# Performance work log

Hardware: AMD Instinct MI355X
Metric: run time of the kernel (lower is better)

The kernel has to match this reference:

```python
import jax, jax.numpy as jnp
from jax import lax
import numpy as np

NUM_INPUTS = 512
NUM_HIDDENS = 1024
BATCH = 64
SEQ_LEN = 512


def setup_inputs() -> dict:
    key = jax.random.key(0)
    ks = jax.random.split(key, 8)
    D, H = NUM_INPUTS, NUM_HIDDENS
    w = lambda k, shape: 0.01 * jax.random.normal(k, shape, dtype=jnp.float32)
    return {
        "inputs": jax.random.normal(ks[0], (BATCH, SEQ_LEN, D), dtype=jnp.float32),
        "state": jax.random.normal(ks[1], (BATCH, H), dtype=jnp.float32),
        "W_xz": w(ks[2], (D, H)), "W_hz": w(ks[3], (H, H)), "b_z": jnp.zeros((H,), jnp.float32),
        "W_xr": w(ks[4], (D, H)), "W_hr": w(ks[5], (H, H)), "b_r": jnp.zeros((H,), jnp.float32),
        "W_xh": w(ks[6], (D, H)), "W_hh": w(ks[7], (H, H)), "b_h": jnp.zeros((H,), jnp.float32),
    }


def reference(inputs, state, W_xz, W_hz, b_z, W_xr, W_hr, b_r, W_xh, W_hh, b_h):
    B, T, _ = inputs.shape
    Hd = state.shape[1]
    # Precompute all input-side gate projections in three big GEMMs: [T, B, H]
    xz = (jnp.einsum('btd,dh->bth', inputs, W_xz) + b_z).transpose(1, 0, 2)
    xr = (jnp.einsum('btd,dh->bth', inputs, W_xr) + b_r).transpose(1, 0, 2)
    xh = (jnp.einsum('btd,dh->bth', inputs, W_xh) + b_h).transpose(1, 0, 2)

    def step(Hc, xs):
        xz_t, xr_t, xh_t = xs
        Z = jax.nn.sigmoid(xz_t + Hc @ W_hz)
        R = jax.nn.sigmoid(xr_t + Hc @ W_hr)
        H_tilda = jnp.tanh(xh_t + (R * Hc) @ W_hh)
        Hn = Z * Hc + (1.0 - Z) * H_tilda
        return Hn, Hn

    H_final, outs = lax.scan(step, state, (xz, xr, xh))  # outs: [T, B, H]
    # torch.cat(outputs, 0) -> [T*B, H]; .transpose(1, 0) -> [H, T*B]
    outputs = outs.reshape(T * B, Hd).T
    return outputs, H_final
```

## Files before the change

kernel.cpp:

```cpp
#include <hip/hip_runtime.h>
#include <hip/hip_bf16.h>

typedef unsigned short ushort_t;
typedef unsigned int uint32;
typedef unsigned long long ull;
typedef short bf16x8 __attribute__((ext_vector_type(8)));
typedef float f32x4 __attribute__((ext_vector_type(4)));

#define Bb 64
#define Tt 512
#define Dd 512
#define Hh 1024
#define KK 1536
#define KP 1544
#define NBLK 64
#define OUT2_OFF 33554432ull
#define FLAGS_OFF 9699328ull
#define XB_OFF    9707776ull
#define XB_BYTES  33554432ull


__device__ inline ushort_t f2b(float f) {
    __hip_bfloat16 h = __float2bfloat16(f);
    return __builtin_bit_cast(ushort_t, h);
}
__device__ inline float b2f(ushort_t u) {
    uint32 x = ((uint32)u) << 16;
    return __builtin_bit_cast(float, x);
}
__device__ inline bf16x8 ld_bf8(const ushort_t* p) {
    uint4 v = *reinterpret_cast<const uint4*>(p);
    return __builtin_bit_cast(bf16x8, v);
}
__device__ inline bf16x8 ld_x8(const float* p) {
    float4 u = *reinterpret_cast<const float4*>(p);
    float4 v = *reinterpret_cast<const float4*>(p + 4);
    bf16x8 a;
    a[0] = (short)f2b(u.x); a[1] = (short)f2b(u.y); a[2] = (short)f2b(u.z); a[3] = (short)f2b(u.w);
    a[4] = (short)f2b(v.x); a[5] = (short)f2b(v.y); a[6] = (short)f2b(v.z); a[7] = (short)f2b(v.w);
    return a;
}
__device__ inline bf16x8 ld_a8(const ushort_t* p) {
    union { ull q[2]; bf16x8 v; } u;
    u.q[0] = __hip_atomic_load((const ull*)p,       __ATOMIC_RELAXED, __HIP_MEMORY_SCOPE_AGENT);
    u.q[1] = __hip_atomic_load((const ull*)(p + 4), __ATOMIC_RELAXED, __HIP_MEMORY_SCOPE_AGENT);
    return u.v;
}
__device__ inline void st_a8(ushort_t* p, ull v) {
    __hip_atomic_store((ull*)p, v, __ATOMIC_RELAXED, __HIP_MEMORY_SCOPE_AGENT);
}

#define MFMA(a, b, c) __builtin_amdgcn_mfma_f32_16x16x32_bf16((a), (b), (c), 0, 0, 0)

__device__ inline void b_arrive(uint32* flags, uint32 val) {
    asm volatile("s_waitcnt vmcnt(0)" ::: "memory");
    __syncthreads();
    if (threadIdx.x == 0)
        __hip_atomic_store(flags + (uint32)blockIdx.x * 32, val,
                           __ATOMIC_RELAXED, __HIP_MEMORY_SCOPE_AGENT);
}
__device__ inline void b_wait(uint32* flags, uint32 val) {
    if (threadIdx.x < 64) {
        uint32 v;
        do {
            v = __hip_atomic_load(flags + threadIdx.x * 32,
                                  __ATOMIC_RELAXED, __HIP_MEMORY_SCOPE_AGENT);
        } while (__any((int)(v < val)));
    }
    __syncthreads();
    asm volatile("" ::: "memory");
}

__global__ __launch_bounds__(256) void k_init(const float* __restrict__ state,
                                              ushort_t* __restrict__ HB, uint32* flags) {
    int i = blockIdx.x * 256 + threadIdx.x;
    if (i < Bb * Hh) HB[i] = f2b(state[i]);
    if (i < 2112) flags[i] = 0;
}

__global__ __launch_bounds__(256) void k_xb(const float* __restrict__ inp,
                                            ushort_t* __restrict__ XB) {
    size_t i = ((size_t)blockIdx.x * 256 + threadIdx.x) * 8;
    bf16x8 v = ld_x8(inp + i);
    *reinterpret_cast<uint4*>(XB + i) = __builtin_bit_cast(uint4, v);
}

__global__ __launch_bounds__(256) void k_wt(const float* __restrict__ Wxz, const float* __restrict__ Whz,
                                            const float* __restrict__ Wxr, const float* __restrict__ Whr,
                                            const float* __restrict__ Wxh, const float* __restrict__ Whh,
                                            ushort_t* __restrict__ WT) {
    __shared__ float lds[64][65];
    int id = blockIdx.x;
    int g = id / 384, rem = id % 384, nt = rem / 24, kt = rem % 24;
    const float* Wx = (g == 0) ? Wxz : (g == 1) ? Wxr : Wxh;
    const float* Wh = (g == 0) ? Whz : (g == 1) ? Whr : Whh;
    int n0 = nt * 64, k0 = kt * 64;
    int tr = threadIdx.x >> 6, tc = threadIdx.x & 63;
    #pragma unroll
    for (int i = 0; i < 16; i++) {
        int kl = i * 4 + tr, k = k0 + kl;
        lds[kl][tc] = (k < 512) ? Wx[(size_t)k * Hh + n0 + tc]
                                : Wh[(size_t)(k - 512) * Hh + n0 + tc];
    }
    __syncthreads();
    #pragma unroll
    for (int i = 0; i < 16; i++) {
        int nl = i * 4 + tr;
        WT[((size_t)g * Hh + n0 + nl) * KK + k0 + tc] = f2b(lds[tc][nl]);
    }
}

__global__ __launch_bounds__(256, 1) void gru_persist(
    const float* __restrict__ inp, const ushort_t* __restrict__ XB, int use_xb,
    const float* __restrict__ bz, const float* __restrict__ br, const float* __restrict__ bh,
    ushort_t* HB, ushort_t* RH, const ushort_t* __restrict__ WT,
    uint32* flags, float* __restrict__ out) {
    __shared__ ushort_t WL[3 * 16 * KP];
    __shared__ ushort_t stage[4][256];

    const int bi = blockIdx.x;
    const int tid = threadIdx.x;

    for (int r = tid >> 4; r < 48; r += 16) {
        const ushort_t* src = WT + ((size_t)(r >> 4) * Hh + bi * 16 + (r & 15)) * KK;
        ushort_t* dst = WL + (size_t)r * KP;
        for (int c = tid & 15; c < 192; c += 16)
            *reinterpret_cast<uint4*>(dst + c * 8) = *reinterpret_cast<const uint4*>(src + c * 8);
    }

    const int l = tid & 63, w = tid >> 6;
    const int lrow = l & 15, lq = l >> 4;
    const int lk8 = lq << 3;

    const int arow = w * 16 + lrow;
    const int brow0 = w * 16 + lq * 4;
    const float*    xbF = inp + (size_t)arow * (Tt * Dd) + lk8;
    const ushort_t* xbB = XB + (size_t)arow * (Tt * Dd) + lk8;
    const ushort_t* hbase = HB + arow * Hh + lk8;
    const ushort_t* rbase = RH + arow * Hh + lk8;
    const int ncol = bi * 16 + lrow;
    const ushort_t* wlz = WL + (0 * 16 + lrow) * KP + lk8;
    const ushort_t* wlr = WL + (1 * 16 + lrow) * KP + lk8;
    const ushort_t* wlh = WL + (2 * 16 + lrow) * KP + lk8;
    const float bzv = bz[ncol], brv = br[ncol], bhv = bh[ncol];

    const size_t strow = (size_t)(w * 16 + (l >> 2)) * Hh + bi * 16 + (l & 3) * 4;
    ushort_t* stW = &stage[w][0];
    const int stw_off = (l >> 2) * 16 + (l & 3) * 4;

    float hold[4];
    #pragma unroll
    for (int j = 0; j < 4; j++) hold[j] = b2f(HB[(size_t)(brow0 + j) * Hh + ncol]);

    __syncthreads();

    for (int t = 0; t < Tt; ++t) {
        bf16x8 xa[16];
        if (use_xb) {
            const ushort_t* xp = xbB + (size_t)t * Dd;
            #pragma unroll
            for (int i = 0; i < 16; i++) xa[i] = ld_bf8(xp + i * 32);
        } else {
            const float* xp = xbF + (size_t)t * Dd;
            #pragma unroll
            for (int i = 0; i < 16; i++) xa[i] = ld_x8(xp + i * 32);
        }

        f32x4 az0 = {0,0,0,0}, az1 = {0,0,0,0}, ar0 = {0,0,0,0}, ar1 = {0,0,0,0};
        f32x4 ah0 = {0,0,0,0}, ah1 = {0,0,0,0}, ah2 = {0,0,0,0}, ah3 = {0,0,0,0};
        #pragma unroll
        for (int kk = 0; kk < 16; kk += 2) {
            const int o = kk * 32;
            az0 = MFMA(xa[kk],     ld_bf8(wlz + o),      az0);
            az1 = MFMA(xa[kk + 1], ld_bf8(wlz + o + 32), az1);
            ar0 = MFMA(xa[kk],     ld_bf8(wlr + o),      ar0);
            ar1 = MFMA(xa[kk + 1], ld_bf8(wlr + o + 32), ar1);
            ah0 = MFMA(xa[kk],     ld_bf8(wlh + o),      ah0);
            ah1 = MFMA(xa[kk + 1], ld_bf8(wlh + o + 32), ah1);
        }

        b_wait(flags, 2u * (uint32)t);

        #pragma unroll
        for (int kk = 0; kk < 32; kk += 2) {
            const int o = kk * 32;
            bf16x8 a0 = ld_a8(hbase + o);
            bf16x8 a1 = ld_a8(hbase + o + 32);
            az0 = MFMA(a0, ld_bf8(wlz + 512 + o),      az0);
            az1 = MFMA(a1, ld_bf8(wlz + 512 + o + 32), az1);
            ar0 = MFMA(a0, ld_bf8(wlr + 512 + o),      ar0);
            ar1 = MFMA(a1, ld_bf8(wlr + 512 + o + 32), ar1);
        }
        f32x4 az = az0 + az1, ar = ar0 + ar1;
        float zreg[4];
        #pragma unroll
        for (int j = 0; j < 4; j++) {
            float zz = 1.f / (1.f + __expf(-(az[j] + bzv)));
            float rr = 1.f / (1.f + __expf(-(ar[j] + brv)));
            zreg[j] = zz;
            stW[(lq * 4 + j) * 16 + lrow] = f2b(rr * hold[j]);
        }
        asm volatile("s_waitcnt lgkmcnt(0)" ::: "memory");
        st_a8(RH + strow, *reinterpret_cast<const ull*>(stW + stw_off));
        b_arrive(flags, 2u * (uint32)t + 1u);
        b_wait(flags, 2u * (uint32)t + 1u);

        #pragma unroll
        for (int kk = 0; kk < 32; kk += 4) {
            const int o = kk * 32;
            bf16x8 a0 = ld_a8(rbase + o);
            bf16x8 a1 = ld_a8(rbase + o + 32);
            bf16x8 a2 = ld_a8(rbase + o + 64);
            bf16x8 a3 = ld_a8(rbase + o + 96);
            ah0 = MFMA(a0, ld_bf8(wlh + 512 + o),      ah0);
            ah1 = MFMA(a1, ld_bf8(wlh + 512 + o + 32), ah1);
            ah2 = MFMA(a2, ld_bf8(wlh + 512 + o + 64), ah2);
            ah3 = MFMA(a3, ld_bf8(wlh + 512 + o + 96), ah3);
        }
        f32x4 ah = (ah0 + ah1) + (ah2 + ah3);
        float hn[4];
        #pragma unroll
        for (int j = 0; j < 4; j++) {
            float pre = ah[j] + bhv;
            float e = __expf(-2.f * fabsf(pre));
            float th = (1.f - e) / (1.f + e);
            th = copysignf(th, pre);
            float v = zreg[j] * hold[j] + (1.f - zreg[j]) * th;
            hold[j] = v;
            hn[j] = v;
            stW[(lq * 4 + j) * 16 + lrow] = f2b(v);
        }
        asm volatile("s_waitcnt lgkmcnt(0)" ::: "memory");
        st_a8(HB + strow, *reinterpret_cast<const ull*>(stW + stw_off));
        *reinterpret_cast<float4*>(out + (size_t)ncol * (Tt * Bb) + (size_t)t * Bb + brow0) =
            make_float4(hn[0], hn[1], hn[2], hn[3]);
        if (t == Tt - 1) {
            #pragma unroll
            for (int j = 0; j < 4; j++)
                out[OUT2_OFF + (size_t)(brow0 + j) * Hh + ncol] = hn[j];
        }
        b_arrive(flags, 2u * (uint32)t + 2u);
    }
}

extern "C" void kernel_launch(void* const* d_in, const int* in_sizes, int n_in,
                              void* d_out, int out_size, void* d_ws, size_t ws_size,
                              hipStream_t stream) {
    const float* inp   = (const float*)d_in[0];
    const float* state = (const float*)d_in[1];
    const float* Wxz   = (const float*)d_in[2];
    const float* Whz   = (const float*)d_in[3];
    const float* bz    = (const float*)d_in[4];
    const float* Wxr   = (const float*)d_in[5];
    const float* Whr   = (const float*)d_in[6];
    const float* br    = (const float*)d_in[7];
    const float* Wxh   = (const float*)d_in[8];
    const float* Whh   = (const float*)d_in[9];
    const float* bh    = (const float*)d_in[10];
    float* out = (float*)d_out;

    char* ws = (char*)d_ws;
    ushort_t* HB    = (ushort_t*)(ws);
    ushort_t* RH    = (ushort_t*)(ws + 131072);
    ushort_t* WT    = (ushort_t*)(ws + 262144);
    uint32*   flags = (uint32*)(ws + FLAGS_OFF);
    ushort_t* XB    = (ushort_t*)(ws + XB_OFF);
    int use_xb = (ws_size >= XB_OFF + XB_BYTES) ? 1 : 0;

    k_init<<<dim3(256), dim3(256), 0, stream>>>(state, HB, flags);
    k_wt<<<dim3(1152), dim3(256), 0, stream>>>(Wxz, Whz, Wxr, Whr, Wxh, Whh, WT);
    if (use_xb)
        k_xb<<<dim3(8192), dim3(256), 0, stream>>>(inp, XB);

    void* args[] = {(void*)&inp, (void*)&XB, (void*)&use_xb,
                    (void*)&bz, (void*)&br, (void*)&bh,
                    (void*)&HB, (void*)&RH, (void*)&WT, (void*)&flags, (void*)&out};
    hipError_t e = hipLaunchCooperativeKernel((const void*)gru_persist, dim3(NBLK), dim3(256),
                                              args, 0, stream);
    if (e != hipSuccess) {
        gru_persist<<<dim3(NBLK), dim3(256), 0, stream>>>(inp, XB, use_xb, bz, br, bh,
                                                          HB, RH, WT, flags, out);
    }
}
```

Measured before the change: 9.811 ms.

## Split K across waves in persistent GRU kernel with LDS cross-wave reduction

Each wave now covers all 64 batch rows over a quarter of the K dimension, instead of 16 rows over the full K. This lets every weight tile read from LDS be reused across four MFMAs, cutting LDS weight traffic. Partial sums are combined through an LDS reduction buffer, which adds extra __syncthreads per step. The weight layout in LDS is also re-tiled with an XOR swizzle to avoid bank conflicts, replacing the padded-row layout.

```diff
diff --git a/kernel.cpp b/kernel.cpp
--- a/kernel.cpp
+++ b/kernel.cpp
@@ -12,7 +12,6 @@
 #define Dd 512
 #define Hh 1024
 #define KK 1536
-#define KP 1544
 #define NBLK 64
 #define OUT2_OFF 33554432ull
 #define FLAGS_OFF 9699328ull
@@ -70,6 +69,23 @@
     __syncthreads();
     asm volatile("" ::: "memory");
 }
+
+#define REDUCE(acc, tot)                                                          \
+    {                                                                             \
+        __syncthreads();                                                          \
+        _Pragma("unroll")                                                         \
+        for (int m_ = 0; m_ < 4; m_++) {                                          \
+            if (m_ != w) {                                                        \
+                int s_ = m_ * 3 + (w < m_ ? w : w - 1);                           \
+                *reinterpret_cast<f32x4*>(&RED[s_ * 256 + l * 4]) = acc[m_];      \
+            }                                                                     \
+        }                                                                         \
+        __syncthreads();                                                          \
+        tot = (w == 0) ? acc[0] : (w == 1) ? acc[1] : (w == 2) ? acc[2] : acc[3]; \
+        _Pragma("unroll")                                                         \
+        for (int i_ = 0; i_ < 3; i_++)                                            \
+            tot += *reinterpret_cast<f32x4*>(&RED[(w * 3 + i_) * 256 + l * 4]);   \
+    }
 
 __global__ __launch_bounds__(256) void k_init(const float* __restrict__ state,
                                               ushort_t* __restrict__ HB, uint32* flags) {
@@ -115,132 +131,157 @@
     const float* __restrict__ bz, const float* __restrict__ br, const float* __restrict__ bh,
     ushort_t* HB, ushort_t* RH, const ushort_t* __restrict__ WT,
     uint32* flags, float* __restrict__ out) {
-    __shared__ ushort_t WL[3 * 16 * KP];
-    __shared__ ushort_t stage[4][256];
+    __shared__ ushort_t WL[3 * 48 * 512];
+    __shared__ float    RED[12 * 256];
+    __shared__ ushort_t STG[4 * 256];
 
     const int bi = blockIdx.x;
     const int tid = threadIdx.x;
 
-    for (int r = tid >> 4; r < 48; r += 16) {
-        const ushort_t* src = WT + ((size_t)(r >> 4) * Hh + bi * 16 + (r & 15)) * KK;
-        ushort_t* dst = WL + (size_t)r * KP;
-        for (int c = tid & 15; c < 192; c += 16)
-            *reinterpret_cast<uint4*>(dst + c * 8) = *reinterpret_cast<const uint4*>(src + c * 8);
+    for (int idx = tid; idx < 9216; idx += 256) {
+        int g = idx / 3072, r = idx % 3072, col = r / 192, c8 = r % 192;
+        int kc = c8 >> 2, slot = c8 & 3, ps = slot ^ ((col >> 1) & 3);
+        const ushort_t* src = WT + ((size_t)g * Hh + bi * 16 + col) * KK + c8 * 8;
+        ushort_t* dst = WL + g * 24576 + kc * 512 + col * 32 + ps * 8;
+        *reinterpret_cast<uint4*>(dst) = *reinterpret_cast<const uint4*>(src);
     }
 
     const int l = tid & 63, w = tid >> 6;
     const int lrow = l & 15, lq = l >> 4;
-    const int lk8 = lq << 3;
-
-    const int arow = w * 16 + lrow;
-    const int brow0 = w * 16 + lq * 4;
-    const float*    xbF = inp + (size_t)arow * (Tt * Dd) + lk8;
-    const ushort_t* xbB = XB + (size_t)arow * (Tt * Dd) + lk8;
-    const ushort_t* hbase = HB + arow * Hh + lk8;
-    const ushort_t* rbase = RH + arow * Hh + lk8;
     const int ncol = bi * 16 + lrow;
-    const ushort_t* wlz = WL + (0 * 16 + lrow) * KP + lk8;
-    const ushort_t* wlr = WL + (1 * 16 + lrow) * KP + lk8;
-    const ushort_t* wlh = WL + (2 * 16 + lrow) * KP + lk8;
+    const int wloff = lrow * 32 + (lq ^ ((lrow >> 1) & 3)) * 8;
     const float bzv = bz[ncol], brv = br[ncol], bhv = bh[ncol];
 
-    const size_t strow = (size_t)(w * 16 + (l >> 2)) * Hh + bi * 16 + (l & 3) * 4;
-    ushort_t* stW = &stage[w][0];
-    const int stw_off = (l >> 2) * 16 + (l & 3) * 4;
+    #define WTILE(g, kc) ld_bf8(WL + (g) * 24576 + (kc) * 512 + wloff)
+
+    const float*    xF[4]; const ushort_t* xB[4];
+    const ushort_t* hb[4]; const ushort_t* rh[4];
+    #pragma unroll
+    for (int m = 0; m < 4; m++) {
+        int row = m * 16 + lrow;
+        xF[m] = inp + (size_t)row * (Tt * Dd) + w * 128 + lq * 8;
+        xB[m] = XB  + (size_t)row * (Tt * Dd) + w * 128 + lq * 8;
+        hb[m] = HB  + row * Hh + w * 256 + lq * 8;
+        rh[m] = RH  + row * Hh + w * 256 + lq * 8;
+    }
+    const size_t strow  = (size_t)(w * 16 + (l >> 2)) * Hh + bi * 16 + (l & 3) * 4;
+    const int    stg_wr = w * 256;
+    const int    stg_rd = w * 256 + (l >> 2) * 16 + (l & 3) * 4;
 
     float hold[4];
     #pragma unroll
-    for (int j = 0; j < 4; j++) hold[j] = b2f(HB[(size_t)(brow0 + j) * Hh + ncol]);
+    for (int j = 0; j < 4; j++)
+        hold[j] = b2f(HB[(size_t)(w * 16 + lq * 4 + j) * Hh + ncol]);
 
     __syncthreads();
 
     for (int t = 0; t < Tt; ++t) {
-        bf16x8 xa[16];
+        const f32x4 z4 = {0.f, 0.f, 0.f, 0.f};
+        f32x4 az[4] = {z4, z4, z4, z4}, ar[4] = {z4, z4, z4, z4}, ahx[4] = {z4, z4, z4, z4};
+
         if (use_xb) {
-            const ushort_t* xp = xbB + (size_t)t * Dd;
-            #pragma unroll
-            for (int i = 0; i < 16; i++) xa[i] = ld_bf8(xp + i * 32);
+            #pragma unroll
+            for (int kk = 0; kk < 4; kk++) {
+                bf16x8 Bz = WTILE(0, w * 4 + kk);
+                bf16x8 Br = WTILE(1, w * 4 + kk);
+                bf16x8 Bh = WTILE(2, w * 4 + kk);
+                #pragma unroll
+                for (int m = 0; m < 4; m++) {
+                    bf16x8 A = ld_bf8(xB[m] + (size_t)t * Dd + kk * 32);
+                    az[m]  = MFMA(A, Bz, az[m]);
+                    ar[m]  = MFMA(A, Br, ar[m]);
+                    ahx[m] = MFMA(A, Bh, ahx[m]);
+                }
+            }
         } else {
-            const float* xp = xbF + (size_t)t * Dd;
-            #pragma unroll
-            for (int i = 0; i < 16; i++) xa[i] = ld_x8(xp + i * 32);
-        }
-
-        f32x4 az0 = {0,0,0,0}, az1 = {0,0,0,0}, ar0 = {0,0,0,0}, ar1 = {0,0,0,0};
-        f32x4 ah0 = {0,0,0,0}, ah1 = {0,0,0,0}, ah2 = {0,0,0,0}, ah3 = {0,0,0,0};
+            #pragma unroll
+            for (int kk = 0; kk < 4; kk++) {
+                bf16x8 Bz = WTILE(0, w * 4 + kk);
+                bf16x8 Br = WTILE(1, w * 4 + kk);
+                bf16x8 Bh = WTILE(2, w * 4 + kk);
+                #pragma unroll
+                for (int m = 0; m < 4; m++) {
+                    bf16x8 A = ld_x8(xF[m] + (size_t)t * Dd + kk * 32);
+                    az[m]  = MFMA(A, Bz, az[m]);
+                    ar[m]  = MFMA(A, Br, ar[m]);
+                    ahx[m] = MFMA(A, Bh, ahx[m]);
+                }
+            }
+        }
+
+        b_wait(flags, 2u * (uint32)t);
+
         #pragma unroll
-        for (int kk = 0; kk < 16; kk += 2) {
-            const int o = kk * 32;
-            az0 = MFMA(xa[kk],     ld_bf8(wlz + o),      az0);
-            az1 = MFMA(xa[kk + 1], ld_bf8(wlz + o + 32), az1);
-            ar0 = MFMA(xa[kk],     ld_bf8(wlr + o),      ar0);
-            ar1 = MFMA(xa[kk + 1], ld_bf8(wlr + o + 32), ar1);
-            ah0 = MFMA(xa[kk],     ld_bf8(wlh + o),      ah0);
-            ah1 = MFMA(xa[kk + 1], ld_bf8(wlh + o + 32), ah1);
-        }
-
-        b_wait(flags, 2u * (uint32)t);
-
-        #pragma unroll
-        for (int kk = 0; kk < 32; kk += 2) {
-            const int o = kk * 32;
-            bf16x8 a0 = ld_a8(hbase + o);
-            bf16x8 a1 = ld_a8(hbase + o + 32);
-            az0 = MFMA(a0, ld_bf8(wlz + 512 + o),      az0);
-            az1 = MFMA(a1, ld_bf8(wlz + 512 + o + 32), az1);
-            ar0 = MFMA(a0, ld_bf8(wlr + 512 + o),      ar0);
-            ar1 = MFMA(a1, ld_bf8(wlr + 512 + o + 32), ar1);
-        }
-        f32x4 az = az0 + az1, ar = ar0 + ar1;
+        for (int kk = 0; kk < 8; kk++) {
+            bf16x8 Bz = WTILE(0, 16 + w * 8 + kk);
+            bf16x8 Br = WTILE(1, 16 + w * 8 + kk);
+            #pragma unroll
+            for (int m = 0; m < 4; m++) {
+                bf16x8 A = ld_a8(hb[m] + kk * 32);
+                az[m] = MFMA(A, Bz, az[m]);
+                ar[m] = MFMA(A, Br, ar[m]);
+            }
+        }
+
+        f32x4 tz, tr;
+        REDUCE(az, tz);
+        REDUCE(ar, tr);
+
         float zreg[4];
         #pragma unroll
         for (int j = 0; j < 4; j++) {
-            float zz = 1.f / (1.f + __expf(-(az[j] + bzv)));
-            float rr = 1.f / (1.f + __expf(-(ar[j] + brv)));
+            float zz = 1.f / (1.f + __expf(-(tz[j] + bzv)));
+            float rr = 1.f / (1.f + __expf(-(tr[j] + brv)));
             zreg[j] = zz;
-            stW[(lq * 4 + j) * 16 + lrow] = f2b(rr * hold[j]);
+            STG[stg_wr + (lq * 4 + j) * 16 + lrow] = f2b(rr * hold[j]);
         }
         asm volatile("s_waitcnt lgkmcnt(0)" ::: "memory");
-        st_a8(RH + strow, *reinterpret_cast<const ull*>(stW + stw_off));
+        st_a8(RH + strow, *reinterpret_cast<const ull*>(&STG[stg_rd]));
+
+        f32x4 thx;
+        REDUCE(ahx, thx);
+
         b_arrive(flags, 2u * (uint32)t + 1u);
         b_wait(flags, 2u * (uint32)t + 1u);
 
+        f32x4 ah[4] = {z4, z4, z4, z4};
         #pragma unroll
-        for (int kk = 0; kk < 32; kk += 4) {
-            const int o = kk * 32;
-            bf16x8 a0 = ld_a8(rbase + o);
-            bf16x8 a1 = ld_a8(rbase + o + 32);
-            bf16x8 a2 = ld_a8(rbase + o + 64);
-            bf16x8 a3 = ld_a8(rbase + o + 96);
-            ah0 = MFMA(a0, ld_bf8(wlh + 512 + o),      ah0);
-            ah1 = MFMA(a1, ld_bf8(wlh + 512 + o + 32), ah1);
-            ah2 = MFMA(a2, ld_bf8(wlh + 512 + o + 64), ah2);
-            ah3 = MFMA(a3, ld_bf8(wlh + 512 + o + 96), ah3);
-        }
-        f32x4 ah = (ah0 + ah1) + (ah2 + ah3);
+        for (int kk = 0; kk < 8; kk++) {
+            bf16x8 Bh = WTILE(2, 16 + w * 8 + kk);
+            #pragma unroll
+            for (int m = 0; m < 4; m++) {
+                bf16x8 A = ld_a8(rh[m] + kk * 32);
+                ah[m] = MFMA(A, Bh, ah[m]);
+            }
+        }
+        f32x4 th4;
+        REDUCE(ah, th4);
+        th4 += thx;
+
         float hn[4];
         #pragma unroll
         for (int j = 0; j < 4; j++) {
-            float pre = ah[j] + bhv;
+            float pre = th4[j] + bhv;
             float e = __expf(-2.f * fabsf(pre));
-            float th = (1.f - e) / (1.f + e);
-            th = copysignf(th, pre);
-            float v = zreg[j] * hold[j] + (1.f - zreg[j]) * th;
+            float v = (1.f - e) / (1.f + e);
+            v = copysignf(v, pre);
+            v = zreg[j] * hold[j] + (1.f - zreg[j]) * v;
             hold[j] = v;
             hn[j] = v;
-            stW[(lq * 4 + j) * 16 + lrow] = f2b(v);
+            STG[stg_wr + (lq * 4 + j) * 16 + lrow] = f2b(v);
         }
         asm volatile("s_waitcnt lgkmcnt(0)" ::: "memory");
-        st_a8(HB + strow, *reinterpret_cast<const ull*>(stW + stw_off));
-        *reinterpret_cast<float4*>(out + (size_t)ncol * (Tt * Bb) + (size_t)t * Bb + brow0) =
+        st_a8(HB + strow, *reinterpret_cast<const ull*>(&STG[stg_rd]));
+        *reinterpret_cast<float4*>(out + (size_t)ncol * (Tt * Bb) + (size_t)t * Bb + w * 16 + lq * 4) =
             make_float4(hn[0], hn[1], hn[2], hn[3]);
         if (t == Tt - 1) {
             #pragma unroll
             for (int j = 0; j < 4; j++)
-                out[OUT2_OFF + (size_t)(brow0 + j) * Hh + ncol] = hn[j];
+                out[OUT2_OFF + (size_t)(w * 16 + lq * 4 + j) * Hh + ncol] = hn[j];
         }
         b_arrive(flags, 2u * (uint32)t + 2u);
     }
+    #undef WTILE
 }
 
 extern "C" void kernel_launch(void* const* d_in, const int* in_sizes, int n_in,
```

Result: slower. 11.00 ms (+12.1%).
